# Kernel optimization log

Measured on AMD Instinct MI355X. Metric: run time of the kernel, lower is better.

Reference implementation:

```python
import jax, jax.numpy as jnp
import numpy as np

K = 3  # kernel_size; padding = 1, stride = 1


def setup_inputs() -> dict:
    key = jax.random.key(0)
    ks = jax.random.split(key, 3)
    b, c, h, w = 8, 96, 256, 256
    x = jax.random.normal(ks[0], (b, c, h, w), dtype=jnp.float32)
    # attention MLP params: 1x1 convs on pooled vector == dense layers
    w1 = jax.random.normal(ks[1], (c // 8, c), dtype=jnp.float32) * (1.0 / np.sqrt(c))
    b1 = jnp.zeros((c // 8,), dtype=jnp.float32)
    w2 = jax.random.normal(ks[2], (K * K, c // 8), dtype=jnp.float32) * (1.0 / np.sqrt(c // 8))
    b2 = jnp.zeros((K * K,), dtype=jnp.float32)
    return {"x": x, "w1": w1, "b1": b1, "w2": w2, "b2": b2}


def reference(x, w1, b1, w2, b2):
    b, c, h, w = x.shape
    # attention: global avg pool -> 1x1 conv -> relu -> 1x1 conv -> softmax over k^2
    pooled = x.mean(axis=(2, 3))                       # (b, c)
    hid = jax.nn.relu(pooled @ w1.T + b1)              # (b, c//8)
    kw = jax.nn.softmax(hid @ w2.T + b2, axis=1)       # (b, k^2), per-batch kernel
    # dynamic depthwise conv: weighted sum of k^2 shifted views (no unfold materialization)
    xp = jnp.pad(x, ((0, 0), (0, 0), (1, 1), (1, 1)))
    out = jnp.zeros_like(x)
    for p in range(K * K):  # F.unfold ordering: row-major over kernel window
        di, dj = p // K, p % K
        out = out + kw[:, p, None, None, None] * xp[:, :, di:di + h, dj:dj + w]
    return out
```

## Files before the change

### kernel.cpp

```cpp
#include <hip/hip_runtime.h>
#include <math.h>


#define NB 8
#define NC 96
#define HH 256
#define WW 256
#define PLANE (HH * WW)
#define NPLANES (NB * NC)

typedef float vfloat4 __attribute__((ext_vector_type(4)));

__global__ __launch_bounds__(256) void pool_kernel(const float* __restrict__ x,
                                                   float* __restrict__ partial) {
    const int blk = blockIdx.x;
    const int tid = threadIdx.x;
    const vfloat4* xp = (const vfloat4*)x + (size_t)(blk >> 2) * (PLANE / 4)
                        + (size_t)(blk & 3) * 4096;
    float s = 0.f;
#pragma unroll
    for (int k = 0; k < 16; ++k) {
        vfloat4 v = xp[k * 256 + tid];
        s += (v.x + v.y) + (v.z + v.w);
    }
#pragma unroll
    for (int off = 32; off > 0; off >>= 1) s += __shfl_down(s, off);
    __shared__ float ws[4];
    if ((tid & 63) == 0) ws[tid >> 6] = s;
    __syncthreads();
    if (tid == 0) partial[blk] = (ws[0] + ws[1]) + (ws[2] + ws[3]);
}

__global__ __launch_bounds__(128) void attn_kernel(const float* __restrict__ partial,
                                                   const float* __restrict__ w1,
                                                   const float* __restrict__ b1,
                                                   const float* __restrict__ w2,
                                                   const float* __restrict__ b2,
                                                   float* __restrict__ kw) {
    const int b = blockIdx.x;
    const int tid = threadIdx.x;
    __shared__ float p[NC];
    __shared__ float hid[12];
    __shared__ float logit[9];
    if (tid < NC) {
        const float* pp = partial + ((size_t)(b * NC + tid) << 2);
        p[tid] = ((pp[0] + pp[1]) + (pp[2] + pp[3])) * (1.0f / (float)PLANE);
    }
    __syncthreads();
    if (tid < 12) {
        float a = b1[tid];
#pragma unroll
        for (int c = 0; c < NC; ++c) a = fmaf(p[c], w1[tid * NC + c], a);
        hid[tid] = a > 0.f ? a : 0.f;
    }
    __syncthreads();
    if (tid < 9) {
        float a = b2[tid];
#pragma unroll
        for (int j = 0; j < 12; ++j) a = fmaf(hid[j], w2[tid * 12 + j], a);
        logit[tid] = a;
    }
    __syncthreads();
    if (tid == 0) {
        float m = logit[0];
#pragma unroll
        for (int q = 1; q < 9; ++q) m = fmaxf(m, logit[q]);
        float e[9], s = 0.f;
#pragma unroll
        for (int q = 0; q < 9; ++q) { e[q] = __expf(logit[q] - m); s += e[q]; }
        float inv = 1.f / s;
#pragma unroll
        for (int q = 0; q < 9; ++q) kw[b * 9 + q] = e[q] * inv;
    }
}

struct Row {
    vfloat4 v;
    float hl, hr;
};

__device__ __forceinline__ vfloat4 raw_row(const float* __restrict__ xpl, int r,
                                           int lane) {
    if ((unsigned)r < (unsigned)HH)
        return *(const vfloat4*)(xpl + (size_t)r * WW + (lane << 2));
    return (vfloat4){0.f, 0.f, 0.f, 0.f};
}

__device__ __forceinline__ Row make_row(vfloat4 v, int lane) {
    Row r;
    r.v = v;
    float up = __shfl_up(v.w, 1);
    float dn = __shfl_down(v.x, 1);
    r.hl = (lane == 0) ? 0.f : up;
    r.hr = (lane == 63) ? 0.f : dn;
    return r;
}

__device__ __forceinline__ void row_fma(const Row& r, float wl, float wc, float wr,
                                        vfloat4& o) {
    o.x = fmaf(wl, r.hl,  fmaf(wc, r.v.x, fmaf(wr, r.v.y, o.x)));
    o.y = fmaf(wl, r.v.x, fmaf(wc, r.v.y, fmaf(wr, r.v.z, o.y)));
    o.z = fmaf(wl, r.v.y, fmaf(wc, r.v.z, fmaf(wr, r.v.w, o.z)));
    o.w = fmaf(wl, r.v.z, fmaf(wc, r.v.w, fmaf(wr, r.hr,  o.w)));
}

__global__ __launch_bounds__(256) void conv_kernel(const float* __restrict__ x,
                                                   const float* __restrict__ kw9,
                                                   float* __restrict__ out) {
    const int lane = threadIdx.x & 63;
    const int strip = (blockIdx.x << 2) + (threadIdx.x >> 6);
    const int rs = strip << 4;

    const size_t base = ((size_t)(blockIdx.z * NC + blockIdx.y)) * PLANE;
    const float* xpl = x + base;
    float* opl = out + base;

    float w[9];
#pragma unroll
    for (int p = 0; p < 9; ++p) w[p] = kw9[blockIdx.z * 9 + p];

    Row a = make_row(raw_row(xpl, rs - 1, lane), lane);
    Row b = make_row(raw_row(xpl, rs, lane), lane);
    vfloat4 pre = raw_row(xpl, rs + 1, lane);

#pragma unroll 4
    for (int i = rs; i < rs + 16; ++i) {
        vfloat4 nxt = (i + 2 <= rs + 16) ? raw_row(xpl, i + 2, lane)
                                         : (vfloat4){0.f, 0.f, 0.f, 0.f};
        Row c = make_row(pre, lane);
        vfloat4 o = (vfloat4){0.f, 0.f, 0.f, 0.f};
        row_fma(a, w[0], w[1], w[2], o);
        row_fma(b, w[3], w[4], w[5], o);
        row_fma(c, w[6], w[7], w[8], o);
        __builtin_nontemporal_store(o, (vfloat4*)(opl + (size_t)i * WW + (lane << 2)));
        a = b; b = c; pre = nxt;
    }
}

extern "C" void kernel_launch(void* const* d_in, const int* in_sizes, int n_in,
                              void* d_out, int out_size, void* d_ws, size_t ws_size,
                              hipStream_t stream) {
    const float* x  = (const float*)d_in[0];
    const float* w1 = (const float*)d_in[1];
    const float* b1 = (const float*)d_in[2];
    const float* w2 = (const float*)d_in[3];
    const float* b2 = (const float*)d_in[4];
    float* out = (float*)d_out;

    float* partial = (float*)d_ws;
    float* kw      = partial + NPLANES * 4;

    pool_kernel<<<NPLANES * 4, 256, 0, stream>>>(x, partial);
    attn_kernel<<<NB, 128, 0, stream>>>(partial, w1, b1, w2, b2, kw);
    dim3 grid(4, NC, NB);
    conv_kernel<<<grid, 256, 0, stream>>>(x, kw, out);
}
```

Baseline: 379.0 us.

## Fuse attention MLP into conv kernel and double rows per strip

Removes the separate attention kernel launch by having each conv block recompute the pooled-vector MLP and softmax into shared memory before its stencil work. The 1/PLANE scaling moves into the pool kernel. Each warp now processes 32 rows instead of 16, which halves the conv grid and amortises the redundant per-block MLP and the halo-row loads. The cost is duplicated MLP work in every block, extra barriers before the stream begins, and fewer blocks available to hide memory latency.

```diff
diff --git a/kernel.cpp b/kernel.cpp
--- a/kernel.cpp
+++ b/kernel.cpp
@@ -28,50 +28,8 @@
     __shared__ float ws[4];
     if ((tid & 63) == 0) ws[tid >> 6] = s;
     __syncthreads();
-    if (tid == 0) partial[blk] = (ws[0] + ws[1]) + (ws[2] + ws[3]);
-}
-
-__global__ __launch_bounds__(128) void attn_kernel(const float* __restrict__ partial,
-                                                   const float* __restrict__ w1,
-                                                   const float* __restrict__ b1,
-                                                   const float* __restrict__ w2,
-                                                   const float* __restrict__ b2,
-                                                   float* __restrict__ kw) {
-    const int b = blockIdx.x;
-    const int tid = threadIdx.x;
-    __shared__ float p[NC];
-    __shared__ float hid[12];
-    __shared__ float logit[9];
-    if (tid < NC) {
-        const float* pp = partial + ((size_t)(b * NC + tid) << 2);
-        p[tid] = ((pp[0] + pp[1]) + (pp[2] + pp[3])) * (1.0f / (float)PLANE);
-    }
-    __syncthreads();
-    if (tid < 12) {
-        float a = b1[tid];
-#pragma unroll
-        for (int c = 0; c < NC; ++c) a = fmaf(p[c], w1[tid * NC + c], a);
-        hid[tid] = a > 0.f ? a : 0.f;
-    }
-    __syncthreads();
-    if (tid < 9) {
-        float a = b2[tid];
-#pragma unroll
-        for (int j = 0; j < 12; ++j) a = fmaf(hid[j], w2[tid * 12 + j], a);
-        logit[tid] = a;
-    }
-    __syncthreads();
-    if (tid == 0) {
-        float m = logit[0];
-#pragma unroll
-        for (int q = 1; q < 9; ++q) m = fmaxf(m, logit[q]);
-        float e[9], s = 0.f;
-#pragma unroll
-        for (int q = 0; q < 9; ++q) { e[q] = __expf(logit[q] - m); s += e[q]; }
-        float inv = 1.f / s;
-#pragma unroll
-        for (int q = 0; q < 9; ++q) kw[b * 9 + q] = e[q] * inv;
-    }
+    if (tid == 0)
+        partial[blk] = ((ws[0] + ws[1]) + (ws[2] + ws[3])) * (1.0f / (float)PLANE);
 }
 
 struct Row {
@@ -105,27 +63,70 @@
 }
 
 __global__ __launch_bounds__(256) void conv_kernel(const float* __restrict__ x,
-                                                   const float* __restrict__ kw9,
+                                                   const float* __restrict__ partial,
+                                                   const float* __restrict__ w1,
+                                                   const float* __restrict__ b1,
+                                                   const float* __restrict__ w2,
+                                                   const float* __restrict__ b2,
                                                    float* __restrict__ out) {
-    const int lane = threadIdx.x & 63;
-    const int strip = (blockIdx.x << 2) + (threadIdx.x >> 6);
-    const int rs = strip << 4;
+    const int tid = threadIdx.x;
+    const int batch = blockIdx.z;
 
-    const size_t base = ((size_t)(blockIdx.z * NC + blockIdx.y)) * PLANE;
-    const float* xpl = x + base;
-    float* opl = out + base;
+    __shared__ float pld[NC];
+    __shared__ float hid[12];
+    __shared__ float lg[9];
+    __shared__ float kwS[9];
+    if (tid < NC) {
+        const float* pp = partial + ((size_t)(batch * NC + tid) << 2);
+        pld[tid] = (pp[0] + pp[1]) + (pp[2] + pp[3]);
+    }
+    __syncthreads();
+    if (tid < 12) {
+        float a = b1[tid];
+#pragma unroll
+        for (int c = 0; c < NC; ++c) a = fmaf(pld[c], w1[tid * NC + c], a);
+        hid[tid] = a > 0.f ? a : 0.f;
+    }
+    __syncthreads();
+    if (tid < 9) {
+        float a = b2[tid];
+#pragma unroll
+        for (int j = 0; j < 12; ++j) a = fmaf(hid[j], w2[tid * 12 + j], a);
+        lg[tid] = a;
+    }
+    __syncthreads();
+    if (tid == 0) {
+        float m = lg[0];
+#pragma unroll
+        for (int q = 1; q < 9; ++q) m = fmaxf(m, lg[q]);
+        float e[9], s = 0.f;
+#pragma unroll
+        for (int q = 0; q < 9; ++q) { e[q] = __expf(lg[q] - m); s += e[q]; }
+        float inv = 1.f / s;
+#pragma unroll
+        for (int q = 0; q < 9; ++q) kwS[q] = e[q] * inv;
+    }
+    __syncthreads();
 
     float w[9];
 #pragma unroll
-    for (int p = 0; p < 9; ++p) w[p] = kw9[blockIdx.z * 9 + p];
+    for (int p = 0; p < 9; ++p) w[p] = kwS[p];
+
+    const int lane = tid & 63;
+    const int strip = (blockIdx.x << 2) + (tid >> 6);
+    const int rs = strip << 5;
+
+    const size_t base = ((size_t)(batch * NC + blockIdx.y)) * PLANE;
+    const float* xpl = x + base;
+    float* opl = out + base;
 
     Row a = make_row(raw_row(xpl, rs - 1, lane), lane);
     Row b = make_row(raw_row(xpl, rs, lane), lane);
     vfloat4 pre = raw_row(xpl, rs + 1, lane);
 
 #pragma unroll 4
-    for (int i = rs; i < rs + 16; ++i) {
-        vfloat4 nxt = (i + 2 <= rs + 16) ? raw_row(xpl, i + 2, lane)
+    for (int i = rs; i < rs + 32; ++i) {
+        vfloat4 nxt = (i + 2 <= rs + 32) ? raw_row(xpl, i + 2, lane)
                                          : (vfloat4){0.f, 0.f, 0.f, 0.f};
         Row c = make_row(pre, lane);
         vfloat4 o = (vfloat4){0.f, 0.f, 0.f, 0.f};
@@ -148,10 +149,8 @@
     float* out = (float*)d_out;
 
     float* partial = (float*)d_ws;
-    float* kw      = partial + NPLANES * 4;
 
     pool_kernel<<<NPLANES * 4, 256, 0, stream>>>(x, partial);
-    attn_kernel<<<NB, 128, 0, stream>>>(partial, w1, b1, w2, b2, kw);
-    dim3 grid(4, NC, NB);
-    conv_kernel<<<grid, 256, 0, stream>>>(x, kw, out);
+    dim3 grid(2, NC, NB);
+    conv_kernel<<<grid, 256, 0, stream>>>(x, partial, w1, b1, w2, b2, out);
 }
```

Result: no change. 379.8 us (+0.2%).
